# Optimization experiments

Measured on AMD Instinct MI355X. Metric: run time of the kernel, lower is better.

## Reference

```python
import jax, jax.numpy as jnp
import numpy as np

MUL = 64                  # multiplicity of 0e and 1o channels
N_NODES = 50000
N_EDGES = 500000
DIM_KEY = 32
FEAT = MUL * 4            # 64x0e (64) + 64x1o (192) = 256
# e3nn FullyConnectedTensorProduct(in, '10x0e', out) normalization:
# path_weight * w3j = 1/sqrt(mul_in * mul_z) = 1/sqrt(64*10)
INV640 = 1.0 / np.sqrt(MUL * 10)
ISQ3 = 1.0 / np.sqrt(3.0)   # w3j(1,1,0) = delta/sqrt(3)
ISQ2 = 1.0 / np.sqrt(2.0)   # path_weight sqrt(alpha) after 'element' norm (2 paths/out)


def _fctp(x, z, W0, W1):
    """FullyConnectedTensorProduct('64x0e+64x1o', '10x0e', '64x0e+64x1o').
    Scalars mix 0e block, vectors mix 1o block; w3j/path-weight factors reduce to 1/sqrt(640)."""
    x0 = x[:, :MUL]                       # (N, 64)
    x1 = x[:, MUL:].reshape(-1, MUL, 3)   # (N, 64, 3)
    o0 = jnp.einsum('nu,nv,uvw->nw', x0, z, W0) * INV640
    o1 = jnp.einsum('nuk,nv,uvw->nwk', x1, z, W1) * INV640
    return jnp.concatenate([o0, o1.reshape(-1, MUL * 3)], axis=-1)


def setup_inputs() -> dict:
    key = jax.random.key(0)
    ks = jax.random.split(key, 13)
    return {
        'x': jax.random.normal(ks[0], (N_NODES, FEAT), jnp.float32),
        'z': jax.random.normal(ks[1], (N_NODES, 10), jnp.float32),
        'edge_src': jax.random.randint(ks[2], (N_EDGES,), 0, N_NODES, jnp.int32),
        'edge_dst': jax.random.randint(ks[3], (N_EDGES,), 0, N_NODES, jnp.int32),
        'edge_len_emb': jax.random.normal(ks[4], (N_EDGES, DIM_KEY), jnp.float32),
        'edge_attr': jax.random.normal(ks[5], (N_EDGES, 4), jnp.float32),
        # learned params: four FCTPs (si, lin1, lin2 each have one 0e and one 1o path)
        'W_si0': jax.random.normal(ks[6], (MUL, 10, MUL), jnp.float32),
        'W_si1': jax.random.normal(ks[7], (MUL, 10, MUL), jnp.float32),
        'W_l1_0': jax.random.normal(ks[8], (MUL, 10, MUL), jnp.float32),
        'W_l1_1': jax.random.normal(ks[9], (MUL, 10, MUL), jnp.float32),
        'W_l2_0': jax.random.normal(ks[10], (MUL, 10, MUL), jnp.float32),
        'W_l2_1': jax.random.normal(ks[11], (MUL, 10, MUL), jnp.float32),
        # per-edge TP weights: 4 'uvu' paths x 64 = 256
        'tp_weight': jax.random.normal(ks[12], (DIM_KEY, 4 * MUL), jnp.float32),
    }


def reference(x, z, edge_src, edge_dst, edge_len_emb, edge_attr,
              W_si0, W_si1, W_l1_0, W_l1_1, W_l2_0, W_l2_1, tp_weight):
    n = x.shape[0]
    s = _fctp(x, z, W_si0, W_si1)          # self-interaction
    xl = _fctp(x, z, W_l1_0, W_l1_1)       # lin1

    w = edge_len_emb @ tp_weight           # (E, 256) per-edge TP weights
    w1, w2, w3, w4 = jnp.split(w, 4, axis=-1)  # instr order: 0ex0e->0e, 0ex1o->1o, 1ox0e->1o, 1ox1o->0e

    xs = xl[edge_src]                      # gather (E, 256)
    x0 = xs[:, :MUL]                       # (E, 64)
    x1 = xs[:, MUL:].reshape(-1, MUL, 3)   # (E, 64, 3)
    sh0 = edge_attr[:, 0:1]                # (E, 1) scalar SH
    sh1 = edge_attr[:, 1:4]                # (E, 3) vector SH

    # 'uvu' weighted tensor product (component norm, element path norm):
    # out_0e = sqrt(1/2) * [ w1*x0*sh0 + w4*(x1.sh1)/sqrt(3) ]
    e0 = ISQ2 * (w1 * x0 * sh0 + ISQ3 * w4 * jnp.einsum('euk,ek->eu', x1, sh1))
    # out_1o = sqrt(3/2)/sqrt(3) * [ w2*x0*sh1 + w3*x1*sh0 ]
    e1 = ISQ2 * (w2[:, :, None] * x0[:, :, None] * sh1[:, None, :]
                 + w3[:, :, None] * x1 * sh0[:, :, None])
    edge_out = jnp.concatenate([e0, e1.reshape(-1, MUL * 3)], axis=-1)  # (E, 256)

    # scatter-add messages to destination nodes
    agg = jnp.zeros((n, FEAT), edge_out.dtype).at[edge_dst].add(edge_out)

    x_out = _fctp(agg, z, W_l2_0, W_l2_1)  # lin2
    return s + x_out / 10
```

## Files before the change

### kernel.cpp

```cpp
#include <hip/hip_runtime.h>

#define MULT 64
#define FEATD 256
#define ZDIM 10

#define INV640f 0.03952847075210474f
#define ISQ2f   0.7071067811865476f
#define ISQ3f   0.5773502691896258f

typedef _Float16 f16_t;
typedef f16_t f16x8_t __attribute__((ext_vector_type(8)));
typedef f16_t f16x4_t __attribute__((ext_vector_type(4)));
typedef float f32x4_t __attribute__((ext_vector_type(4)));

__global__ __launch_bounds__(256) void transform_x2(
    const float* __restrict__ x, f16_t* __restrict__ Xs,
    f16_t* __restrict__ Xv, int N)
{
    int idx = blockIdx.x * 256 + threadIdx.x;
    if (idx >= N * MULT) return;
    int n = idx >> 6;
    int u = idx & 63;
    const float* row = x + (size_t)n * FEATD;
    Xs[idx] = (f16_t)row[u];
    const float* x1p = row + MULT + u * 3;
    Xv[((size_t)3 * n + 0) * MULT + u] = (f16_t)x1p[0];
    Xv[((size_t)3 * n + 1) * MULT + u] = (f16_t)x1p[1];
    Xv[((size_t)3 * n + 2) * MULT + u] = (f16_t)x1p[2];
}

__global__ __launch_bounds__(256) void zprep_kernel(
    const float* __restrict__ z, float* __restrict__ zt,
    float* __restrict__ ztv, int N)
{
    int n = blockIdx.x * 256 + threadIdx.x;
    if (n >= N) return;
    const float* zr = z + (size_t)n * ZDIM;
#pragma unroll
    for (int v = 0; v < ZDIM; ++v) {
        float val = zr[v] * INV640f;
        zt[(size_t)v * N + n] = val;
        float* p = ztv + (size_t)v * 3 * N + 3 * (size_t)n;
        p[0] = val; p[1] = val; p[2] = val;
    }
}

__global__ __launch_bounds__(256) void tpwprep_kernel(
    const float* __restrict__ tpw, f16_t* __restrict__ tpwt)
{
    int idx = blockIdx.x * 256 + threadIdx.x;
    if (idx >= 256 * 32) return;
    int c = idx >> 5, k = idx & 31;
    float s = (c < 192) ? ISQ2f : (ISQ2f * ISQ3f);
    tpwt[(size_t)c * 32 + k] = (f16_t)(tpw[(size_t)k * 256 + c] * s);
}

__global__ __launch_bounds__(256) void aggcvt_kernel(
    const float* __restrict__ a, f16_t* __restrict__ h, int n4)
{
    int i = blockIdx.x * 256 + threadIdx.x;
    if (i >= n4) return;
    float4 v = *(const float4*)(a + (size_t)i * 4);
    f16x4_t o;
    o[0] = (f16_t)v.x; o[1] = (f16_t)v.y; o[2] = (f16_t)v.z; o[3] = (f16_t)v.w;
    *(f16x4_t*)(h + (size_t)i * 4) = o;
}

__device__ __forceinline__ void preload_W(
    const float* __restrict__ W, int c0, int q, int mm, f16x8_t (&B)[20])
{
    const int col = c0 + mm;
#pragma unroll
    for (int ks = 0; ks < 20; ++ks) {
        const int v = ks >> 1;
        const int ub = ((ks & 1) << 5) + (q << 3);
        const int base = v * 64 + col;
#pragma unroll
        for (int j = 0; j < 8; ++j)
            B[ks][j] = (f16_t)W[(ub + j) * 640 + base];
    }
}

__global__ __launch_bounds__(256, 2) void fctp_pass_out(
    const f16_t* __restrict__ Xs, const f16_t* __restrict__ Xv,
    const float* __restrict__ zt, const float* __restrict__ ztv,
    const float* __restrict__ Wsi0, const float* __restrict__ Wsi1,
    float* __restrict__ out, int N, int nsc)
{
    const int lane = threadIdx.x & 63;
    const int wave = threadIdx.x >> 6;
    const int c0 = wave << 4;
    const int q = lane >> 4;
    const int mm = lane & 15;
    const bool sc = (int)blockIdx.x < nsc;
    const float* W = sc ? Wsi0 : Wsi1;
    const f16_t* Xsel = sc ? Xs : Xv;
    const float* ztb = sc ? zt : ztv;
    const size_t zsr = sc ? (size_t)N : (size_t)3 * N;
    const int ntiles = sc ? (N >> 4) : ((3 * N) >> 4);
    const int worker = sc ? (int)blockIdx.x : ((int)blockIdx.x - nsc);
    const int nworkers = sc ? nsc : 3 * nsc;

    f16x8_t B[20];
    preload_W(W, c0, q, mm, B);

    int tile = worker;
    if (tile >= ntiles) return;
    f16x8_t cxlo, cxhi;
    f32x4_t czq[ZDIM];
    {
        const int r = (tile << 4) + mm;
        cxlo = *(const f16x8_t*)(Xsel + ((size_t)r << 6) + (q << 3));
        cxhi = *(const f16x8_t*)(Xsel + ((size_t)r << 6) + 32 + (q << 3));
        const int rb4 = (tile << 4) + (q << 2);
#pragma unroll
        for (int v = 0; v < ZDIM; ++v)
            czq[v] = *(const f32x4_t*)(ztb + (size_t)v * zsr + rb4);
    }

    for (; tile < ntiles; tile += nworkers) {
        const int nt = tile + nworkers;
        f16x8_t nxlo = cxlo, nxhi = cxhi;
        f32x4_t nzq[ZDIM];
#pragma unroll
        for (int v = 0; v < ZDIM; ++v) nzq[v] = czq[v];
        if (nt < ntiles) {
            const int r = (nt << 4) + mm;
            nxlo = *(const f16x8_t*)(Xsel + ((size_t)r << 6) + (q << 3));
            nxhi = *(const f16x8_t*)(Xsel + ((size_t)r << 6) + 32 + (q << 3));
            const int nrb4 = (nt << 4) + (q << 2);
#pragma unroll
            for (int v = 0; v < ZDIM; ++v)
                nzq[v] = *(const f32x4_t*)(ztb + (size_t)v * zsr + nrb4);
        }
        __builtin_amdgcn_sched_barrier(0);

        const int rb4 = (tile << 4) + (q << 2);
        f32x4_t acc = {0.f, 0.f, 0.f, 0.f};
#pragma unroll
        for (int v = 0; v < ZDIM; ++v) {
            f32x4_t t = {0.f, 0.f, 0.f, 0.f};
            t = __builtin_amdgcn_mfma_f32_16x16x32_f16(cxlo, B[2 * v], t, 0, 0, 0);
            t = __builtin_amdgcn_mfma_f32_16x16x32_f16(cxhi, B[2 * v + 1], t, 0, 0, 0);
#pragma unroll
            for (int reg = 0; reg < 4; ++reg)
                acc[reg] = fmaf(czq[v][reg], t[reg], acc[reg]);
        }

        const int w = c0 + mm;
#pragma unroll
        for (int reg = 0; reg < 4; ++reg) {
            const int ro = rb4 + reg;
            if (sc) {
                out[(size_t)ro * FEATD + w] = acc[reg];
            } else {
                const unsigned nn = (unsigned)ro / 3u;
                const int k = ro - 3 * (int)nn;
                out[(size_t)nn * FEATD + MULT + w * 3 + k] = acc[reg];
            }
        }
        cxlo = nxlo; cxhi = nxhi;
#pragma unroll
        for (int v = 0; v < ZDIM; ++v) czq[v] = nzq[v];
    }
}

__global__ __launch_bounds__(256, 2) void fctp_pass_xl(
    const f16_t* __restrict__ Xs, const f16_t* __restrict__ Xv,
    const float* __restrict__ zt, const float* __restrict__ ztv,
    const float* __restrict__ Wl10, const float* __restrict__ Wl11,
    f16_t* __restrict__ xls, f16_t* __restrict__ xlv, int N, int nsc)
{
    const int lane = threadIdx.x & 63;
    const int wave = threadIdx.x >> 6;
    const int c0 = wave << 4;
    const int q = lane >> 4;
    const int mm = lane & 15;
    const bool sc = (int)blockIdx.x < nsc;
    const float* W = sc ? Wl10 : Wl11;
    const f16_t* Xsel = sc ? Xs : Xv;
    const float* ztb = sc ? zt : ztv;
    const size_t zsr = sc ? (size_t)N : (size_t)3 * N;
    const int ntiles = sc ? (N >> 4) : ((3 * N) >> 4);
    const int worker = sc ? (int)blockIdx.x : ((int)blockIdx.x - nsc);
    const int nworkers = sc ? nsc : 3 * nsc;

    f16x8_t B[20];
    preload_W(W, c0, q, mm, B);

    f16_t* Osel = sc ? xls : xlv;

    int tile = worker;
    if (tile >= ntiles) return;
    f16x8_t cxlo, cxhi;
    f32x4_t czq[ZDIM];
    {
        const int r = (tile << 4) + mm;
        cxlo = *(const f16x8_t*)(Xsel + ((size_t)r << 6) + (q << 3));
        cxhi = *(const f16x8_t*)(Xsel + ((size_t)r << 6) + 32 + (q << 3));
        const int rb4 = (tile << 4) + (q << 2);
#pragma unroll
        for (int v = 0; v < ZDIM; ++v)
            czq[v] = *(const f32x4_t*)(ztb + (size_t)v * zsr + rb4);
    }

    for (; tile < ntiles; tile += nworkers) {
        const int nt = tile + nworkers;
        f16x8_t nxlo = cxlo, nxhi = cxhi;
        f32x4_t nzq[ZDIM];
#pragma unroll
        for (int v = 0; v < ZDIM; ++v) nzq[v] = czq[v];
        if (nt < ntiles) {
            const int r = (nt << 4) + mm;
            nxlo = *(const f16x8_t*)(Xsel + ((size_t)r << 6) + (q << 3));
            nxhi = *(const f16x8_t*)(Xsel + ((size_t)r << 6) + 32 + (q << 3));
            const int nrb4 = (nt << 4) + (q << 2);
#pragma unroll
            for (int v = 0; v < ZDIM; ++v)
                nzq[v] = *(const f32x4_t*)(ztb + (size_t)v * zsr + nrb4);
        }
        __builtin_amdgcn_sched_barrier(0);

        const int rb4 = (tile << 4) + (q << 2);
        f32x4_t acc = {0.f, 0.f, 0.f, 0.f};
#pragma unroll
        for (int v = 0; v < ZDIM; ++v) {
            f32x4_t t = {0.f, 0.f, 0.f, 0.f};
            t = __builtin_amdgcn_mfma_f32_16x16x32_f16(cxlo, B[2 * v], t, 0, 0, 0);
            t = __builtin_amdgcn_mfma_f32_16x16x32_f16(cxhi, B[2 * v + 1], t, 0, 0, 0);
#pragma unroll
            for (int reg = 0; reg < 4; ++reg)
                acc[reg] = fmaf(czq[v][reg], t[reg], acc[reg]);
        }

        const int w = c0 + mm;
#pragma unroll
        for (int reg = 0; reg < 4; ++reg) {
            const int ro = rb4 + reg;
            Osel[((size_t)ro << 6) + w] = (f16_t)acc[reg];
        }
        cxlo = nxlo; cxhi = nxhi;
#pragma unroll
        for (int v = 0; v < ZDIM; ++v) czq[v] = nzq[v];
    }
}

__global__ __launch_bounds__(256, 2) void fctp_stageC_mfma(
    const f16_t* __restrict__ aggsh, const f16_t* __restrict__ aggvh,
    const float* __restrict__ zt, const float* __restrict__ ztv,
    const float* __restrict__ Wl20, const float* __restrict__ Wl21,
    float* __restrict__ out, int N, int nsc)
{
    const int lane = threadIdx.x & 63;
    const int wave = threadIdx.x >> 6;
    const int c0 = wave << 4;
    const int q = lane >> 4;
    const int mm = lane & 15;
    const bool sc = (int)blockIdx.x < nsc;
    const float* W = sc ? Wl20 : Wl21;
    const f16_t* Asel = sc ? aggsh : aggvh;
    const float* ztb = sc ? zt : ztv;
    const size_t zsr = sc ? (size_t)N : (size_t)3 * N;
    const int ntiles = sc ? (N >> 4) : ((3 * N) >> 4);
    const int worker = sc ? (int)blockIdx.x : ((int)blockIdx.x - nsc);
    const int nworkers = sc ? nsc : 3 * nsc;

    f16x8_t B[20];
    preload_W(W, c0, q, mm, B);

    int tile = worker;
    if (tile >= ntiles) return;
    f16x8_t cxlo, cxhi;
    f32x4_t czq[ZDIM];
    {
        const int r = (tile << 4) + mm;
        cxlo = *(const f16x8_t*)(Asel + ((size_t)r << 6) + (q << 3));
        cxhi = *(const f16x8_t*)(Asel + ((size_t)r << 6) + 32 + (q << 3));
        const int rb4 = (tile << 4) + (q << 2);
#pragma unroll
        for (int v = 0; v < ZDIM; ++v)
            czq[v] = *(const f32x4_t*)(ztb + (size_t)v * zsr + rb4);
    }

    for (; tile < ntiles; tile += nworkers) {
        const int nt = tile + nworkers;
        f16x8_t nxlo = cxlo, nxhi = cxhi;
        f32x4_t nzq[ZDIM];
#pragma unroll
        for (int v = 0; v < ZDIM; ++v) nzq[v] = czq[v];
        if (nt < ntiles) {
            const int r = (nt << 4) + mm;
            nxlo = *(const f16x8_t*)(Asel + ((size_t)r << 6) + (q << 3));
            nxhi = *(const f16x8_t*)(Asel + ((size_t)r << 6) + 32 + (q << 3));
            const int nrb4 = (nt << 4) + (q << 2);
#pragma unroll
            for (int v = 0; v < ZDIM; ++v)
                nzq[v] = *(const f32x4_t*)(ztb + (size_t)v * zsr + nrb4);
        }
        const int rb4 = (tile << 4) + (q << 2);
        const int w = c0 + mm;
        size_t oidx[4];
        float oold[4];
#pragma unroll
        for (int reg = 0; reg < 4; ++reg) {
            const int ro = rb4 + reg;
            if (sc) {
                oidx[reg] = (size_t)ro * FEATD + w;
            } else {
                const unsigned nn = (unsigned)ro / 3u;
                const int k = ro - 3 * (int)nn;
                oidx[reg] = (size_t)nn * FEATD + MULT + w * 3 + k;
            }
            oold[reg] = out[oidx[reg]];
        }
        __builtin_amdgcn_sched_barrier(0);

        f32x4_t acc = {0.f, 0.f, 0.f, 0.f};
#pragma unroll
        for (int v = 0; v < ZDIM; ++v) {
            f32x4_t t = {0.f, 0.f, 0.f, 0.f};
            t = __builtin_amdgcn_mfma_f32_16x16x32_f16(cxlo, B[2 * v], t, 0, 0, 0);
            t = __builtin_amdgcn_mfma_f32_16x16x32_f16(cxhi, B[2 * v + 1], t, 0, 0, 0);
#pragma unroll
            for (int reg = 0; reg < 4; ++reg)
                acc[reg] = fmaf(czq[v][reg], t[reg], acc[reg]);
        }

#pragma unroll
        for (int reg = 0; reg < 4; ++reg)
            out[oidx[reg]] = oold[reg] + acc[reg] * 0.1f;

        cxlo = nxlo; cxhi = nxhi;
#pragma unroll
        for (int v = 0; v < ZDIM; ++v) czq[v] = nzq[v];
    }
}

__global__ __launch_bounds__(256) void hist_kernel(
    const int* __restrict__ edst, int* __restrict__ cnt, int E)
{
    int e = blockIdx.x * 256 + threadIdx.x;
    if (e >= E) return;
    atomicAdd(&cnt[edst[e]], 1);
}

__global__ __launch_bounds__(1024) void scan_block(
    const int* __restrict__ cnt, int* __restrict__ off,
    int* __restrict__ bsum, int N)
{
    __shared__ int sh[1024];
    int tid = threadIdx.x;
    int i = blockIdx.x * 1024 + tid;
    int v = (i < N) ? cnt[i] : 0;
    sh[tid] = v;
    __syncthreads();
#pragma unroll
    for (int d = 1; d < 1024; d <<= 1) {
        int t = (tid >= d) ? sh[tid - d] : 0;
        __syncthreads();
        sh[tid] += t;
        __syncthreads();
    }
    if (i < N) off[i + 1] = sh[tid];
    if (tid == 1023) bsum[blockIdx.x] = sh[1023];
    if (i == 0) off[0] = 0;
}

__global__ __launch_bounds__(64) void scan_sums(int* __restrict__ bsum, int nb)
{
    int tid = threadIdx.x;
    int v = (tid < nb) ? bsum[tid] : 0;
#pragma unroll
    for (int d = 1; d < 64; d <<= 1) {
        int t = __shfl_up(v, d, 64);
        if (tid >= d) v += t;
    }
    int ex = __shfl_up(v, 1, 64);
    if (tid == 0) ex = 0;
    if (tid < nb) bsum[tid] = ex;
}

__global__ __launch_bounds__(1024) void scan_add(
    int* __restrict__ off, const int* __restrict__ bsum, int N)
{
    int i = blockIdx.x * 1024 + threadIdx.x;
    if (i < N) off[i + 1] += bsum[blockIdx.x];
}

__global__ __launch_bounds__(256) void scatter_kernel(
    const int* __restrict__ edst, const int* __restrict__ esrc,
    const float* __restrict__ eattr, const int* __restrict__ off,
    int* __restrict__ cursor, int* __restrict__ perm,
    int* __restrict__ sperm, float* __restrict__ eattr_p, int E)
{
    int e = blockIdx.x * 256 + threadIdx.x;
    if (e >= E) return;
    int d = edst[e];
    int pos = off[d] + atomicAdd(&cursor[d], 1);
    perm[pos] = e;
    sperm[pos] = esrc[e];
    float4 at = *(const float4*)(eattr + (size_t)e * 4);
    *(float4*)(eattr_p + (size_t)pos * 4) = at;
}

__global__ __launch_bounds__(256, 2) void wgemm_kernel(
    const int* __restrict__ perm, const float* __restrict__ elem,
    const f16_t* __restrict__ tpwt, f16_t* __restrict__ wbuf,
    int lo, int ntiles)
{
    const int lane = threadIdx.x & 63;
    const int mm = lane & 15, q = lane >> 4;
    int tile = blockIdx.x * 4 + (threadIdx.x >> 6);
    const int nw = gridDim.x * 4;

    f16x8_t B[16];
#pragma unroll
    for (int s = 0; s < 16; ++s)
        B[s] = *(const f16x8_t*)(tpwt + ((size_t)(s * 16 + mm)) * 32 + q * 8);

    if (tile >= ntiles) return;
    float4 ca, cb;
    {
        int e = perm[lo + (tile << 4) + mm];
        const float* er = elem + ((size_t)e << 5) + q * 8;
        ca = *(const float4*)er;
        cb = *(const float4*)(er + 4);
    }

    for (; tile < ntiles; tile += nw) {
        const int nt = tile + nw;
        float4 na = ca, nb = cb;
        if (nt < ntiles) {
            int e = perm[lo + (nt << 4) + mm];
            const float* er = elem + ((size_t)e << 5) + q * 8;
            na = *(const float4*)er;
            nb = *(const float4*)(er + 4);
        }

        f16x8_t A;
        A[0] = (f16_t)ca.x; A[1] = (f16_t)ca.y; A[2] = (f16_t)ca.z; A[3] = (f16_t)ca.w;
        A[4] = (f16_t)cb.x; A[5] = (f16_t)cb.y; A[6] = (f16_t)cb.z; A[7] = (f16_t)cb.w;

        f32x4_t D[16];
#pragma unroll
        for (int s = 0; s < 16; ++s) {
            f32x4_t zer = {0.f, 0.f, 0.f, 0.f};
            D[s] = __builtin_amdgcn_mfma_f32_16x16x32_f16(A, B[s], zer, 0, 0, 0);
        }

#pragma unroll
        for (int reg = 0; reg < 4; ++reg) {
            const int row = q * 4 + reg;
            const size_t base = ((size_t)((tile << 4) + row)) << 6;
#pragma unroll
            for (int t = 0; t < 4; ++t) {
                const int u = t * 16 + mm;
                f16x4_t wq;
                wq[0] = (f16_t)D[0 * 4 + t][reg];
                wq[1] = (f16_t)D[1 * 4 + t][reg];
                wq[2] = (f16_t)D[2 * 4 + t][reg];
                wq[3] = (f16_t)D[3 * 4 + t][reg];
                *(f16x4_t*)(wbuf + ((base + u) << 2)) = wq;
            }
        }
        ca = na; cb = nb;
    }
}

__device__ __forceinline__ void agg_edge5(
    float xs, float v0, float v1, float v2, int i, int lo,
    const f16_t* __restrict__ wbuf, const float* __restrict__ eattr_p, int u,
    float& accx, float& accy, float& accz, float& accw)
{
    f16x4_t wq = *(const f16x4_t*)(wbuf + ((((size_t)(i - lo)) << 6) + u) * 4);
    float w1 = (float)wq[0], w2 = (float)wq[1], w3 = (float)wq[2], w4 = (float)wq[3];
    float4 at = *(const float4*)(eattr_p + ((size_t)i << 2));
    float dot3 = v0 * at.y + v1 * at.z + v2 * at.w;
    accx = fmaf(w1 * xs, at.x, accx);
    accx = fmaf(w4, dot3, accx);
    float w2x = w2 * xs;
    accy = fmaf(w2x, at.y, accy);
    accz = fmaf(w2x, at.z, accz);
    accw = fmaf(w2x, at.w, accw);
    float w3s = w3 * at.x;
    accy = fmaf(w3s, v0, accy);
    accz = fmaf(w3s, v1, accz);
    accw = fmaf(w3s, v2, accw);
}

__global__ __launch_bounds__(256, 8) void aggregate5(
    const int* __restrict__ off, const int* __restrict__ sperm,
    const f16_t* __restrict__ wbuf, const float* __restrict__ eattr_p,
    const f16_t* __restrict__ xls, const f16_t* __restrict__ xlv,
    float* __restrict__ aggs, float* __restrict__ aggv,
    int N, int lo, int hi)
{
    int n = (blockIdx.x * 256 + threadIdx.x) >> 6;
    if (n >= N) return;
    int u = threadIdx.x & 63;

    int s0 = __builtin_amdgcn_readfirstlane(off[n]);
    int s1 = __builtin_amdgcn_readfirstlane(off[n + 1]);
    int cs0 = s0 > lo ? s0 : lo;
    int cs1 = s1 < hi ? s1 : hi;
    if (cs0 >= cs1) return;

    float accx = 0.f, accy = 0.f, accz = 0.f, accw = 0.f;
    const int last = cs1 - 1;

    int sa = __builtin_amdgcn_readfirstlane(sperm[cs0]);
    float a_xs = (float)xls[((size_t)sa << 6) + u];
    float a_v0 = (float)xlv[((size_t)(3 * sa + 0) << 6) + u];
    float a_v1 = (float)xlv[((size_t)(3 * sa + 1) << 6) + u];
    float a_v2 = (float)xlv[((size_t)(3 * sa + 2) << 6) + u];
    int ib = (cs0 + 1 <= last) ? cs0 + 1 : last;
    int sb = __builtin_amdgcn_readfirstlane(sperm[ib]);
    float b_xs = (float)xls[((size_t)sb << 6) + u];
    float b_v0 = (float)xlv[((size_t)(3 * sb + 0) << 6) + u];
    float b_v1 = (float)xlv[((size_t)(3 * sb + 1) << 6) + u];
    float b_v2 = (float)xlv[((size_t)(3 * sb + 2) << 6) + u];

    int i = cs0;
    while (true) {
        agg_edge5(a_xs, a_v0, a_v1, a_v2, i, lo, wbuf, eattr_p, u,
                  accx, accy, accz, accw);
        {
            int inx = (i + 2 <= last) ? i + 2 : last;
            int sn = __builtin_amdgcn_readfirstlane(sperm[inx]);
            a_xs = (float)xls[((size_t)sn << 6) + u];
            a_v0 = (float)xlv[((size_t)(3 * sn + 0) << 6) + u];
            a_v1 = (float)xlv[((size_t)(3 * sn + 1) << 6) + u];
            a_v2 = (float)xlv[((size_t)(3 * sn + 2) << 6) + u];
        }
        if (++i > last) break;
        agg_edge5(b_xs, b_v0, b_v1, b_v2, i, lo, wbuf, eattr_p, u,
                  accx, accy, accz, accw);
        {
            int inx = (i + 2 <= last) ? i + 2 : last;
            int sn = __builtin_amdgcn_readfirstlane(sperm[inx]);
            b_xs = (float)xls[((size_t)sn << 6) + u];
            b_v0 = (float)xlv[((size_t)(3 * sn + 0) << 6) + u];
            b_v1 = (float)xlv[((size_t)(3 * sn + 1) << 6) + u];
            b_v2 = (float)xlv[((size_t)(3 * sn + 2) << 6) + u];
        }
        if (++i > last) break;
    }

    aggs[((size_t)n << 6) + u] += accx;
    aggv[((size_t)(3 * n + 0) << 6) + u] += accy;
    aggv[((size_t)(3 * n + 1) << 6) + u] += accz;
    aggv[((size_t)(3 * n + 2) << 6) + u] += accw;
}

extern "C" void kernel_launch(void* const* d_in, const int* in_sizes, int n_in,
                              void* d_out, int out_size, void* d_ws, size_t ws_size,
                              hipStream_t stream)
{
    const float* x     = (const float*)d_in[0];
    const float* z     = (const float*)d_in[1];
    const int*   esrc  = (const int*)d_in[2];
    const int*   edst  = (const int*)d_in[3];
    const float* elem  = (const float*)d_in[4];
    const float* eattr = (const float*)d_in[5];
    const float* Wsi0  = (const float*)d_in[6];
    const float* Wsi1  = (const float*)d_in[7];
    const float* Wl10  = (const float*)d_in[8];
    const float* Wl11  = (const float*)d_in[9];
    const float* Wl20  = (const float*)d_in[10];
    const float* Wl21  = (const float*)d_in[11];
    const float* tpw   = (const float*)d_in[12];
    float* out = (float*)d_out;

    const int N = in_sizes[1] / ZDIM;
    const int E = in_sizes[2];
    const int Ehalf = E / 2;

    f16_t* xls  = (f16_t*)d_ws;
    f16_t* xlv  = xls + (size_t)N * 64;
    float* aggs = (float*)(xlv + (size_t)3 * N * 64);
    float* aggv = aggs + (size_t)N * 64;
    char*  R    = (char*)(aggv + (size_t)3 * N * 64);
    f16_t* Xs   = (f16_t*)R;
    f16_t* Xv   = Xs + (size_t)N * 64;
    f16_t* wbuf = (f16_t*)R;
    f16_t* aggh = (f16_t*)R;
    size_t Rbytes = (size_t)Ehalf * 256 * sizeof(f16_t);
    float* eattr_p = (float*)(R + Rbytes);
    int*   sperm   = (int*)(eattr_p + (size_t)E * 4);
    int*   perm    = sperm + E;
    int*   cnt     = perm + E;
    int*   cursor  = cnt + N;
    int*   off     = cursor + N;
    int*   bsum    = off + (N + 1);
    size_t zoff = (((size_t)(bsum + 64) - (size_t)d_ws) + 255) & ~(size_t)255;
    float* zt  = (float*)((char*)d_ws + zoff);
    float* ztv = zt + (size_t)10 * N;
    f16_t* tpwt = (f16_t*)(ztv + (size_t)30 * N);

    const int SCAN_B = 1024;
    int nb = (N + SCAN_B - 1) / SCAN_B;

    hipMemsetAsync(cnt, 0, 2 * (size_t)N * sizeof(int), stream);
    hipMemsetAsync(aggs, 0, (size_t)4 * N * 64 * sizeof(float), stream);

    int g0 = (N * MULT + 255) / 256;
    hipLaunchKernelGGL(transform_x2, dim3(g0), dim3(256), 0, stream, x, Xs, Xv, N);
    int gz = (N + 255) / 256;
    hipLaunchKernelGGL(zprep_kernel, dim3(gz), dim3(256), 0, stream, z, zt, ztv, N);
    hipLaunchKernelGGL(tpwprep_kernel, dim3(32), dim3(256), 0, stream, tpw, tpwt);

    hipLaunchKernelGGL(fctp_pass_xl, dim3(512), dim3(256), 0, stream,
                       Xs, Xv, zt, ztv, Wl10, Wl11, xls, xlv, N, 128);
    hipLaunchKernelGGL(fctp_pass_out, dim3(512), dim3(256), 0, stream,
                       Xs, Xv, zt, ztv, Wsi0, Wsi1, out, N, 128);

    int geh = (E + 255) / 256;
    hipLaunchKernelGGL(hist_kernel, dim3(geh), dim3(256), 0, stream,
                       edst, cnt, E);
    hipLaunchKernelGGL(scan_block, dim3(nb), dim3(SCAN_B), 0, stream,
                       cnt, off, bsum, N);
    hipLaunchKernelGGL(scan_sums, dim3(1), dim3(64), 0, stream, bsum, nb);
    hipLaunchKernelGGL(scan_add, dim3(nb), dim3(SCAN_B), 0, stream,
                       off, bsum, N);
    hipLaunchKernelGGL(scatter_kernel, dim3(geh), dim3(256), 0, stream,
                       edst, esrc, eattr, off, cursor, perm, sperm, eattr_p, E);

    int wt = Ehalf / 16;
    int ga = (N * 64 + 255) / 256;
    for (int c = 0; c < 2; ++c) {
        int lo = c * Ehalf, hi = lo + Ehalf;
        hipLaunchKernelGGL(wgemm_kernel, dim3(512), dim3(256), 0, stream,
                           perm, elem, tpwt, wbuf, lo, wt);
        hipLaunchKernelGGL(aggregate5, dim3(ga), dim3(256), 0, stream,
                           off, sperm, wbuf, eattr_p, xls, xlv,
                           aggs, aggv, N, lo, hi);
    }

    int n4 = N * 64;
    int gc = (n4 + 255) / 256;
    hipLaunchKernelGGL(aggcvt_kernel, dim3(gc), dim3(256), 0, stream,
                       aggs, aggh, n4);
    hipLaunchKernelGGL(fctp_stageC_mfma, dim3(512), dim3(256), 0, stream,
                       aggh, aggh + (size_t)N * 64, zt, ztv, Wl20, Wl21,
                       out, N, 128);
}
```

Before: 553.0 us.

## Fuse per-edge weight GEMM into aggregation kernel via LDS tiles

Removes the separate wgemm pass that wrote per-edge f16 TP weights to a global buffer in two half-edge chunks. Each wavefront now computes the weights for 16 of its node's edges at a time with MFMA into LDS and consumes them right away. This drops the global write and read of the weight buffer, the two-chunk loop, and the memset of the aggregation buffers, since results are now stored directly. In exchange the kernel needs 32KB of LDS per block and has occupancy bounded at 3. Nodes with few edges still pay a full 16-row MFMA tile, so some matrix work is wasted, and there is no explicit wave sync between the LDS writes and reads.

```diff
diff --git a/kernel.cpp b/kernel.cpp
--- a/kernel.cpp
+++ b/kernel.cpp
@@ -403,153 +403,138 @@
     *(float4*)(eattr_p + (size_t)pos * 4) = at;
 }
 
-__global__ __launch_bounds__(256, 2) void wgemm_kernel(
+__global__ __launch_bounds__(256, 3) void aggregate6(
+    const int* __restrict__ off, const int* __restrict__ sperm,
     const int* __restrict__ perm, const float* __restrict__ elem,
-    const f16_t* __restrict__ tpwt, f16_t* __restrict__ wbuf,
-    int lo, int ntiles)
-{
-    const int lane = threadIdx.x & 63;
-    const int mm = lane & 15, q = lane >> 4;
-    int tile = blockIdx.x * 4 + (threadIdx.x >> 6);
-    const int nw = gridDim.x * 4;
+    const f16_t* __restrict__ tpwt, const float* __restrict__ eattr_p,
+    const f16_t* __restrict__ xls, const f16_t* __restrict__ xlv,
+    float* __restrict__ aggs, float* __restrict__ aggv, int N)
+{
+    __shared__ f16_t wtile[4][16 * 256];
+    int n = (blockIdx.x * 256 + threadIdx.x) >> 6;
+    if (n >= N) return;
+    const int u = threadIdx.x & 63;
+    const int wid = threadIdx.x >> 6;
+    const int mm = u & 15, q = u >> 4;
+    f16_t* wt = &wtile[wid][0];
 
     f16x8_t B[16];
 #pragma unroll
     for (int s = 0; s < 16; ++s)
         B[s] = *(const f16x8_t*)(tpwt + ((size_t)(s * 16 + mm)) * 32 + q * 8);
 
-    if (tile >= ntiles) return;
-    float4 ca, cb;
-    {
-        int e = perm[lo + (tile << 4) + mm];
-        const float* er = elem + ((size_t)e << 5) + q * 8;
-        ca = *(const float4*)er;
-        cb = *(const float4*)(er + 4);
-    }
-
-    for (; tile < ntiles; tile += nw) {
-        const int nt = tile + nw;
-        float4 na = ca, nb = cb;
-        if (nt < ntiles) {
-            int e = perm[lo + (nt << 4) + mm];
+    int cs0 = __builtin_amdgcn_readfirstlane(off[n]);
+    int cs1 = __builtin_amdgcn_readfirstlane(off[n + 1]);
+
+    float accx = 0.f, accy = 0.f, accz = 0.f, accw = 0.f;
+
+    if (cs0 < cs1) {
+        const int last = cs1 - 1;
+
+        int sa = __builtin_amdgcn_readfirstlane(sperm[cs0]);
+        float a_xs = (float)xls[((size_t)sa << 6) + u];
+        float a_v0 = (float)xlv[((size_t)(3 * sa + 0) << 6) + u];
+        float a_v1 = (float)xlv[((size_t)(3 * sa + 1) << 6) + u];
+        float a_v2 = (float)xlv[((size_t)(3 * sa + 2) << 6) + u];
+        int ib = (cs0 + 1 <= last) ? cs0 + 1 : last;
+        int sb = __builtin_amdgcn_readfirstlane(sperm[ib]);
+        float b_xs = (float)xls[((size_t)sb << 6) + u];
+        float b_v0 = (float)xlv[((size_t)(3 * sb + 0) << 6) + u];
+        float b_v1 = (float)xlv[((size_t)(3 * sb + 1) << 6) + u];
+        float b_v2 = (float)xlv[((size_t)(3 * sb + 2) << 6) + u];
+
+        int i = cs0;
+        for (int g = cs0; g < cs1; g += 16) {
+            const int gend = (g + 16 < cs1) ? g + 16 : cs1;
+
+            int pos = g + mm; if (pos > last) pos = last;
+            int e = perm[pos];
             const float* er = elem + ((size_t)e << 5) + q * 8;
-            na = *(const float4*)er;
-            nb = *(const float4*)(er + 4);
-        }
-
-        f16x8_t A;
-        A[0] = (f16_t)ca.x; A[1] = (f16_t)ca.y; A[2] = (f16_t)ca.z; A[3] = (f16_t)ca.w;
-        A[4] = (f16_t)cb.x; A[5] = (f16_t)cb.y; A[6] = (f16_t)cb.z; A[7] = (f16_t)cb.w;
-
-        f32x4_t D[16];
-#pragma unroll
-        for (int s = 0; s < 16; ++s) {
-            f32x4_t zer = {0.f, 0.f, 0.f, 0.f};
-            D[s] = __builtin_amdgcn_mfma_f32_16x16x32_f16(A, B[s], zer, 0, 0, 0);
-        }
-
-#pragma unroll
-        for (int reg = 0; reg < 4; ++reg) {
-            const int row = q * 4 + reg;
-            const size_t base = ((size_t)((tile << 4) + row)) << 6;
+            float4 ea = *(const float4*)er;
+            float4 eb = *(const float4*)(er + 4);
+            f16x8_t A;
+            A[0] = (f16_t)ea.x; A[1] = (f16_t)ea.y; A[2] = (f16_t)ea.z; A[3] = (f16_t)ea.w;
+            A[4] = (f16_t)eb.x; A[5] = (f16_t)eb.y; A[6] = (f16_t)eb.z; A[7] = (f16_t)eb.w;
+
 #pragma unroll
             for (int t = 0; t < 4; ++t) {
-                const int u = t * 16 + mm;
-                f16x4_t wq;
-                wq[0] = (f16_t)D[0 * 4 + t][reg];
-                wq[1] = (f16_t)D[1 * 4 + t][reg];
-                wq[2] = (f16_t)D[2 * 4 + t][reg];
-                wq[3] = (f16_t)D[3 * 4 + t][reg];
-                *(f16x4_t*)(wbuf + ((base + u) << 2)) = wq;
+                f32x4_t D0 = {0.f, 0.f, 0.f, 0.f}, D1 = {0.f, 0.f, 0.f, 0.f};
+                f32x4_t D2 = {0.f, 0.f, 0.f, 0.f}, D3 = {0.f, 0.f, 0.f, 0.f};
+                D0 = __builtin_amdgcn_mfma_f32_16x16x32_f16(A, B[t],      D0, 0, 0, 0);
+                D1 = __builtin_amdgcn_mfma_f32_16x16x32_f16(A, B[4 + t],  D1, 0, 0, 0);
+                D2 = __builtin_amdgcn_mfma_f32_16x16x32_f16(A, B[8 + t],  D2, 0, 0, 0);
+                D3 = __builtin_amdgcn_mfma_f32_16x16x32_f16(A, B[12 + t], D3, 0, 0, 0);
+#pragma unroll
+                for (int reg = 0; reg < 4; ++reg) {
+                    const int row = (q << 2) + reg;
+                    f16x4_t wq;
+                    wq[0] = (f16_t)D0[reg];
+                    wq[1] = (f16_t)D1[reg];
+                    wq[2] = (f16_t)D2[reg];
+                    wq[3] = (f16_t)D3[reg];
+                    *(f16x4_t*)(wt + ((size_t)(row * 64 + (t * 16 + mm)) << 2)) = wq;
+                }
             }
-        }
-        ca = na; cb = nb;
-    }
-}
-
-__device__ __forceinline__ void agg_edge5(
-    float xs, float v0, float v1, float v2, int i, int lo,
-    const f16_t* __restrict__ wbuf, const float* __restrict__ eattr_p, int u,
-    float& accx, float& accy, float& accz, float& accw)
-{
-    f16x4_t wq = *(const f16x4_t*)(wbuf + ((((size_t)(i - lo)) << 6) + u) * 4);
-    float w1 = (float)wq[0], w2 = (float)wq[1], w3 = (float)wq[2], w4 = (float)wq[3];
-    float4 at = *(const float4*)(eattr_p + ((size_t)i << 2));
-    float dot3 = v0 * at.y + v1 * at.z + v2 * at.w;
-    accx = fmaf(w1 * xs, at.x, accx);
-    accx = fmaf(w4, dot3, accx);
-    float w2x = w2 * xs;
-    accy = fmaf(w2x, at.y, accy);
-    accz = fmaf(w2x, at.z, accz);
-    accw = fmaf(w2x, at.w, accw);
-    float w3s = w3 * at.x;
-    accy = fmaf(w3s, v0, accy);
-    accz = fmaf(w3s, v1, accz);
-    accw = fmaf(w3s, v2, accw);
-}
-
-__global__ __launch_bounds__(256, 8) void aggregate5(
-    const int* __restrict__ off, const int* __restrict__ sperm,
-    const f16_t* __restrict__ wbuf, const float* __restrict__ eattr_p,
-    const f16_t* __restrict__ xls, const f16_t* __restrict__ xlv,
-    float* __restrict__ aggs, float* __restrict__ aggv,
-    int N, int lo, int hi)
-{
-    int n = (blockIdx.x * 256 + threadIdx.x) >> 6;
-    if (n >= N) return;
-    int u = threadIdx.x & 63;
-
-    int s0 = __builtin_amdgcn_readfirstlane(off[n]);
-    int s1 = __builtin_amdgcn_readfirstlane(off[n + 1]);
-    int cs0 = s0 > lo ? s0 : lo;
-    int cs1 = s1 < hi ? s1 : hi;
-    if (cs0 >= cs1) return;
-
-    float accx = 0.f, accy = 0.f, accz = 0.f, accw = 0.f;
-    const int last = cs1 - 1;
-
-    int sa = __builtin_amdgcn_readfirstlane(sperm[cs0]);
-    float a_xs = (float)xls[((size_t)sa << 6) + u];
-    float a_v0 = (float)xlv[((size_t)(3 * sa + 0) << 6) + u];
-    float a_v1 = (float)xlv[((size_t)(3 * sa + 1) << 6) + u];
-    float a_v2 = (float)xlv[((size_t)(3 * sa + 2) << 6) + u];
-    int ib = (cs0 + 1 <= last) ? cs0 + 1 : last;
-    int sb = __builtin_amdgcn_readfirstlane(sperm[ib]);
-    float b_xs = (float)xls[((size_t)sb << 6) + u];
-    float b_v0 = (float)xlv[((size_t)(3 * sb + 0) << 6) + u];
-    float b_v1 = (float)xlv[((size_t)(3 * sb + 1) << 6) + u];
-    float b_v2 = (float)xlv[((size_t)(3 * sb + 2) << 6) + u];
-
-    int i = cs0;
-    while (true) {
-        agg_edge5(a_xs, a_v0, a_v1, a_v2, i, lo, wbuf, eattr_p, u,
-                  accx, accy, accz, accw);
-        {
-            int inx = (i + 2 <= last) ? i + 2 : last;
-            int sn = __builtin_amdgcn_readfirstlane(sperm[inx]);
-            a_xs = (float)xls[((size_t)sn << 6) + u];
-            a_v0 = (float)xlv[((size_t)(3 * sn + 0) << 6) + u];
-            a_v1 = (float)xlv[((size_t)(3 * sn + 1) << 6) + u];
-            a_v2 = (float)xlv[((size_t)(3 * sn + 2) << 6) + u];
-        }
-        if (++i > last) break;
-        agg_edge5(b_xs, b_v0, b_v1, b_v2, i, lo, wbuf, eattr_p, u,
-                  accx, accy, accz, accw);
-        {
-            int inx = (i + 2 <= last) ? i + 2 : last;
-            int sn = __builtin_amdgcn_readfirstlane(sperm[inx]);
-            b_xs = (float)xls[((size_t)sn << 6) + u];
-            b_v0 = (float)xlv[((size_t)(3 * sn + 0) << 6) + u];
-            b_v1 = (float)xlv[((size_t)(3 * sn + 1) << 6) + u];
-            b_v2 = (float)xlv[((size_t)(3 * sn + 2) << 6) + u];
-        }
-        if (++i > last) break;
-    }
-
-    aggs[((size_t)n << 6) + u] += accx;
-    aggv[((size_t)(3 * n + 0) << 6) + u] += accy;
-    aggv[((size_t)(3 * n + 1) << 6) + u] += accz;
-    aggv[((size_t)(3 * n + 2) << 6) + u] += accw;
+
+            while (i < gend) {
+                {
+                    f16x4_t wq = *(const f16x4_t*)(wt + ((size_t)((i - g) * 64 + u) << 2));
+                    float w1 = (float)wq[0], w2 = (float)wq[1], w3 = (float)wq[2], w4 = (float)wq[3];
+                    float4 at = *(const float4*)(eattr_p + ((size_t)i << 2));
+                    float dot3 = a_v0 * at.y + a_v1 * at.z + a_v2 * at.w;
+                    accx = fmaf(w1 * a_xs, at.x, accx);
+                    accx = fmaf(w4, dot3, accx);
+                    float w2x = w2 * a_xs;
+                    accy = fmaf(w2x, at.y, accy);
+                    accz = fmaf(w2x, at.z, accz);
+                    accw = fmaf(w2x, at.w, accw);
+                    float w3s = w3 * at.x;
+                    accy = fmaf(w3s, a_v0, accy);
+                    accz = fmaf(w3s, a_v1, accz);
+                    accw = fmaf(w3s, a_v2, accw);
+                }
+                {
+                    int inx = (i + 2 <= last) ? i + 2 : last;
+                    int sn = __builtin_amdgcn_readfirstlane(sperm[inx]);
+                    a_xs = (float)xls[((size_t)sn << 6) + u];
+                    a_v0 = (float)xlv[((size_t)(3 * sn + 0) << 6) + u];
+                    a_v1 = (float)xlv[((size_t)(3 * sn + 1) << 6) + u];
+                    a_v2 = (float)xlv[((size_t)(3 * sn + 2) << 6) + u];
+                }
+                if (++i >= gend) break;
+                {
+                    f16x4_t wq = *(const f16x4_t*)(wt + ((size_t)((i - g) * 64 + u) << 2));
+                    float w1 = (float)wq[0], w2 = (float)wq[1], w3 = (float)wq[2], w4 = (float)wq[3];
+                    float4 at = *(const float4*)(eattr_p + ((size_t)i << 2));
+                    float dot3 = b_v0 * at.y + b_v1 * at.z + b_v2 * at.w;
+                    accx = fmaf(w1 * b_xs, at.x, accx);
+                    accx = fmaf(w4, dot3, accx);
+                    float w2x = w2 * b_xs;
+                    accy = fmaf(w2x, at.y, accy);
+                    accz = fmaf(w2x, at.z, accz);
+                    accw = fmaf(w2x, at.w, accw);
+                    float w3s = w3 * at.x;
+                    accy = fmaf(w3s, b_v0, accy);
+                    accz = fmaf(w3s, b_v1, accz);
+                    accw = fmaf(w3s, b_v2, accw);
+                }
+                {
+                    int inx = (i + 2 <= last) ? i + 2 : last;
+                    int sn = __builtin_amdgcn_readfirstlane(sperm[inx]);
+                    b_xs = (float)xls[((size_t)sn << 6) + u];
+                    b_v0 = (float)xlv[((size_t)(3 * sn + 0) << 6) + u];
+                    b_v1 = (float)xlv[((size_t)(3 * sn + 1) << 6) + u];
+                    b_v2 = (float)xlv[((size_t)(3 * sn + 2) << 6) + u];
+                }
+                ++i;
+            }
+        }
+    }
+
+    aggs[((size_t)n << 6) + u] = accx;
+    aggv[((size_t)(3 * n + 0) << 6) + u] = accy;
+    aggv[((size_t)(3 * n + 1) << 6) + u] = accz;
+    aggv[((size_t)(3 * n + 2) << 6) + u] = accw;
 }
 
 extern "C" void kernel_launch(void* const* d_in, const int* in_sizes, int n_in,
@@ -582,7 +567,6 @@
     char*  R    = (char*)(aggv + (size_t)3 * N * 64);
     f16_t* Xs   = (f16_t*)R;
     f16_t* Xv   = Xs + (size_t)N * 64;
-    f16_t* wbuf = (f16_t*)R;
     f16_t* aggh = (f16_t*)R;
     size_t Rbytes = (size_t)Ehalf * 256 * sizeof(f16_t);
     float* eattr_p = (float*)(R + Rbytes);
@@ -601,7 +585,6 @@
     int nb = (N + SCAN_B - 1) / SCAN_B;
 
     hipMemsetAsync(cnt, 0, 2 * (size_t)N * sizeof(int), stream);
-    hipMemsetAsync(aggs, 0, (size_t)4 * N * 64 * sizeof(float), stream);
 
     int g0 = (N * MULT + 255) / 256;
     hipLaunchKernelGGL(transform_x2, dim3(g0), dim3(256), 0, stream, x, Xs, Xv, N);
@@ -625,16 +608,10 @@
     hipLaunchKernelGGL(scatter_kernel, dim3(geh), dim3(256), 0, stream,
                        edst, esrc, eattr, off, cursor, perm, sperm, eattr_p, E);
 
-    int wt = Ehalf / 16;
     int ga = (N * 64 + 255) / 256;
-    for (int c = 0; c < 2; ++c) {
-        int lo = c * Ehalf, hi = lo + Ehalf;
-        hipLaunchKernelGGL(wgemm_kernel, dim3(512), dim3(256), 0, stream,
-                           perm, elem, tpwt, wbuf, lo, wt);
-        hipLaunchKernelGGL(aggregate5, dim3(ga), dim3(256), 0, stream,
-                           off, sperm, wbuf, eattr_p, xls, xlv,
-                           aggs, aggv, N, lo, hi);
-    }
+    hipLaunchKernelGGL(aggregate6, dim3(ga), dim3(256), 0, stream,
+                       off, sperm, perm, elem, tpwt, eattr_p, xls, xlv,
+                       aggs, aggv, N);
 
     int n4 = N * 64;
     int gc = (n4 + 255) / 256;
```

Measured after the change: 508.7 us. -8.0%, faster.
